# Performance work log

Measured on AMD Instinct MI355X. Metric: run time of the kernel, lower is better.

## Reference

```python
import jax, jax.numpy as jnp
import numpy as np

N = 500000      # examples = M * (nr+1)
K = 20          # context set size (indices[:, 3:])
NR = 24         # negatives per positive
H = 128         # hidden_channels == node feature dim
NODES = 10000   # ingredient vocabulary


def setup_inputs() -> dict:
    key = jax.random.key(0)
    ks = jax.random.split(key, 6)
    indices = jax.random.randint(ks[0], (N, 3 + K), 0, NODES)
    x = jax.random.normal(ks[1], (NODES, H), dtype=jnp.float32)
    scale = 0.02
    W1 = jax.random.normal(ks[2], (H, 3 * H), dtype=jnp.float32) * scale
    b1 = jnp.zeros((H,), jnp.float32)
    W2 = jax.random.normal(ks[3], (H // 2, H), dtype=jnp.float32) * scale
    b2 = jnp.zeros((H // 2,), jnp.float32)
    W3 = jax.random.normal(ks[4], (1, H // 2), dtype=jnp.float32) * scale
    b3 = jnp.zeros((1,), jnp.float32)
    return {"indices": indices, "nr": NR, "x": x,
            "W1": W1, "b1": b1, "W2": W2, "b2": b2, "W3": W3, "b3": b3}


def _embed_context(ctx_idx, x, nr):
    # ctx_idx: [N, K]; one context row per group of (nr+1) examples
    new_idx = ctx_idx[:-1:nr + 1]                 # [M, K]
    emb = x[new_idx]                               # [M, K, H] gather
    s = emb.sum(axis=1)                            # [M, H]
    norm = jnp.maximum((new_idx > 0).sum(axis=1), 1).astype(x.dtype)[:, None]
    mean = s / norm                                # masked mean over context
    return jnp.repeat(mean, nr + 1, axis=0)        # broadcast back to [N, H]


def reference(indices, nr, x, W1, b1, W2, b2, W3, b3):
    ing1 = x[indices[:, 0]]                        # [N, H]
    ing2 = x[indices[:, 1]]                        # [N, H]
    set_emb = _embed_context(indices[:, 3:], x, nr)  # [N, H]
    y = jnp.concatenate([ing1, ing2, set_emb], axis=1)  # [N, 3H]
    y = jax.nn.relu(y @ W1.T + b1)
    y = jax.nn.relu(y @ W2.T + b2)
    return y @ W3.T + b3                           # [N, 1]
```

## Files before the change

### kernel.cpp

```cpp
#include <hip/hip_runtime.h>
#include <hip/hip_bf16.h>

#define N_ROWS   500000
#define NR1      25
#define NGROUPS  20000
#define KCTX     20
#define H        128
#define NODES    10000
#define IDX_COLS 23

#define RPB      128
#define MAXG     7

typedef __attribute__((ext_vector_type(8))) short short8;
typedef __attribute__((ext_vector_type(4))) float f32x4;

__device__ __forceinline__ unsigned pkbf(float lo, float hi) {
  __hip_bfloat162 h = __float22bfloat162_rn(make_float2(lo, hi));
  union { __hip_bfloat162 h; unsigned u; } c; c.h = h;
  return c.u;
}
__device__ __forceinline__ float bf2f(unsigned short u) {
  union { unsigned u; float f; } c; c.u = ((unsigned)u) << 16; return c.f;
}

#define PN 64
#define PRE_BLOCKS ((NODES + PN - 1) / PN)
__global__ __launch_bounds__(256) void k_precompute(
    const float* __restrict__ x, const float* __restrict__ W1,
    const int* __restrict__ indices,
    unsigned short* __restrict__ Pb, int2* __restrict__ idx2) {
  const int tid = threadIdx.x;
  const int m   = blockIdx.y;

  if (m == 3) {
    const int stride = PRE_BLOCKS * 256;
    for (int r = blockIdx.x * 256 + tid; r < N_ROWS; r += stride) {
      idx2[r] = make_int2(indices[(size_t)r * IDX_COLS + 0],
                          indices[(size_t)r * IDX_COLS + 1]);
    }
    return;
  }

  __shared__ short wlds[128][136];
  const int tbase = blockIdx.x * PN;

#pragma unroll
  for (int it = 0; it < 16; ++it) {
    const int f  = it * 256 + tid;
    const int j  = f >> 5;
    const int q4 = f & 31;
    const float4 v = *(const float4*)(W1 + (size_t)j * (3 * H) + m * H + q4 * 4);
    *(unsigned*)&wlds[j][q4 * 4]     = pkbf(v.x, v.y);
    *(unsigned*)&wlds[j][q4 * 4 + 2] = pkbf(v.z, v.w);
  }
  __syncthreads();

  const int lane = tid & 63;
  const int wv   = tid >> 6;
  const int col  = lane & 15;
  const int quad = lane >> 4;

  int node = tbase + wv * 16 + col;
  if (node > NODES - 1) node = NODES - 1;
  const float4* __restrict__ xr = (const float4*)(x + (size_t)node * H);

  short8 Af[4];
#pragma unroll
  for (int kt = 0; kt < 4; ++kt) {
    const int f4 = kt * 8 + quad * 2;
    const float4 v0 = xr[f4], v1 = xr[f4 + 1];
    union { short8 v; unsigned u[4]; } pk;
    pk.u[0] = pkbf(v0.x, v0.y);
    pk.u[1] = pkbf(v0.z, v0.w);
    pk.u[2] = pkbf(v1.x, v1.y);
    pk.u[3] = pkbf(v1.z, v1.w);
    Af[kt] = pk.v;
  }

  f32x4 acc[8];
#pragma unroll
  for (int ct = 0; ct < 8; ++ct) acc[ct] = (f32x4)(0.f);

#pragma unroll
  for (int kt = 0; kt < 4; ++kt) {
#pragma unroll
    for (int ct = 0; ct < 8; ++ct) {
      const short8 Bf = *(const short8*)&wlds[ct * 16 + col][kt * 32 + quad * 8];
      acc[ct] = __builtin_amdgcn_mfma_f32_16x16x32_bf16(Af[kt], Bf, acc[ct], 0, 0, 0);
    }
  }

  unsigned short* __restrict__ Pm = Pb + (size_t)m * NODES * H;
#pragma unroll
  for (int reg = 0; reg < 4; ++reg) {
    const int n = tbase + wv * 16 + quad * 4 + reg;
    if (n < NODES) {
#pragma unroll
      for (int ct = 0; ct < 8; ++ct) {
        union { unsigned u; unsigned short s[2]; } c;
        c.u = pkbf(acc[ct][reg], 0.f);
        Pm[(size_t)n * H + ct * 16 + col] = c.s[0];
      }
    }
  }
}

__global__ __launch_bounds__(256) void k_main(
    const int* __restrict__ indices, const int2* __restrict__ idx2,
    const unsigned short* __restrict__ P1b, const unsigned short* __restrict__ P2b,
    const unsigned short* __restrict__ P3b,
    const float* __restrict__ W2, const float* __restrict__ b1,
    const float* __restrict__ b2, const float* __restrict__ W3,
    const float* __restrict__ b3, float* __restrict__ out) {
  __shared__ short w2s[64][136];
  __shared__ float cgs[MAXG][132];

  const int tid   = threadIdx.x;
  const int rbase = blockIdx.x * RPB;
  const int gbase = rbase / NR1;

  const int lane = tid & 63;
  const int wv   = tid >> 6;
  const int col  = lane & 15;
  const int quad = lane >> 4;

  short8 ua[2][4], ub[2][4];
  int    gl[2];
  {
    const int R = rbase + wv * 32;
#pragma unroll
    for (int rt = 0; rt < 2; ++rt) {
      const int r  = R + rt * 16 + col;
      const int rc = (r < N_ROWS) ? r : (N_ROWS - 1);
      const int2 ii = idx2[rc];
      const short8* __restrict__ pa = (const short8*)(P1b + (size_t)ii.x * H);
      const short8* __restrict__ pb = (const short8*)(P2b + (size_t)ii.y * H);
#pragma unroll
      for (int kt = 0; kt < 4; ++kt) {
        ua[rt][kt] = pa[kt * 4 + quad];
        ub[rt][kt] = pb[kt * 4 + quad];
      }
      gl[rt] = rc / NR1 - gbase;
    }
  }

  for (int idx = tid; idx < 64 * 64; idx += 256) {
    const int n  = idx >> 6;
    const int kp = idx & 63;
    const float2 w = *(const float2*)(W2 + (size_t)n * H + kp * 2);
    *(unsigned*)&w2s[n][kp * 2] = pkbf(w.x, w.y);
  }

  {
    int rlast = rbase + RPB - 1; if (rlast > N_ROWS - 1) rlast = N_ROWS - 1;
    const int G   = rlast / NR1 - gbase + 1;
    const int jj  = (tid & 63) * 2;
    const int sub = tid >> 6;
    const float2 b1v = *(const float2*)(b1 + jj);
#pragma unroll
    for (int it = 0; it < 2; ++it) {
      const int gi = it * 4 + sub;
      if (gi < G) {
        const int* __restrict__ rowidx =
            indices + (size_t)(gbase + gi) * NR1 * IDX_COLS + 3;
        float s0 = 0.f, s1 = 0.f;
        int cnt = 0;
#pragma unroll
        for (int c = 0; c < KCTX; ++c) {
          const int idx = rowidx[c];
          const unsigned w = *(const unsigned*)(P3b + (size_t)idx * H + jj);
          s0 += bf2f((unsigned short)(w & 0xffffu));
          s1 += bf2f((unsigned short)(w >> 16));
          cnt += (idx > 0) ? 1 : 0;
        }
        const float rn = 1.f / (float)((cnt > 1) ? cnt : 1);
        cgs[gi][jj]     = b1v.x + s0 * rn;
        cgs[gi][jj + 1] = b1v.y + s1 * rn;
      }
    }
  }
  __syncthreads();

  float b2v[4], w3v[4];
#pragma unroll
  for (int ct = 0; ct < 4; ++ct) {
    b2v[ct] = b2[ct * 16 + col];
    w3v[ct] = W3[ct * 16 + col];
  }
  const float bias3 = b3[0];

  short8 A[2][4];
#pragma unroll
  for (int rt = 0; rt < 2; ++rt) {
#pragma unroll
    for (int kt = 0; kt < 4; ++kt) {
      union { short8 v; unsigned short s[8]; } va, vb;
      va.v = ua[rt][kt];
      vb.v = ub[rt][kt];
      const float4 c0 = *(const float4*)&cgs[gl[rt]][kt * 32 + quad * 8];
      const float4 c1 = *(const float4*)&cgs[gl[rt]][kt * 32 + quad * 8 + 4];
      const float h0 = fmaxf(bf2f(va.s[0]) + bf2f(vb.s[0]) + c0.x, 0.f);
      const float h1 = fmaxf(bf2f(va.s[1]) + bf2f(vb.s[1]) + c0.y, 0.f);
      const float h2 = fmaxf(bf2f(va.s[2]) + bf2f(vb.s[2]) + c0.z, 0.f);
      const float h3 = fmaxf(bf2f(va.s[3]) + bf2f(vb.s[3]) + c0.w, 0.f);
      const float h4 = fmaxf(bf2f(va.s[4]) + bf2f(vb.s[4]) + c1.x, 0.f);
      const float h5 = fmaxf(bf2f(va.s[5]) + bf2f(vb.s[5]) + c1.y, 0.f);
      const float h6 = fmaxf(bf2f(va.s[6]) + bf2f(vb.s[6]) + c1.z, 0.f);
      const float h7 = fmaxf(bf2f(va.s[7]) + bf2f(vb.s[7]) + c1.w, 0.f);
      union { short8 v; unsigned u[4]; } pk;
      pk.u[0] = pkbf(h0, h1);
      pk.u[1] = pkbf(h2, h3);
      pk.u[2] = pkbf(h4, h5);
      pk.u[3] = pkbf(h6, h7);
      A[rt][kt] = pk.v;
    }
  }

  f32x4 acc[2][4];
#pragma unroll
  for (int rt = 0; rt < 2; ++rt)
#pragma unroll
    for (int ct = 0; ct < 4; ++ct) acc[rt][ct] = (f32x4)(0.f);
#pragma unroll
  for (int kt = 0; kt < 4; ++kt) {
#pragma unroll
    for (int ct = 0; ct < 4; ++ct) {
      const short8 Bf = *(const short8*)&w2s[ct * 16 + col][kt * 32 + quad * 8];
#pragma unroll
      for (int rt = 0; rt < 2; ++rt)
        acc[rt][ct] = __builtin_amdgcn_mfma_f32_16x16x32_bf16(
            A[rt][kt], Bf, acc[rt][ct], 0, 0, 0);
    }
  }

  const int Rt = rbase + wv * 32;
#pragma unroll
  for (int rt = 0; rt < 2; ++rt) {
#pragma unroll
    for (int reg = 0; reg < 4; ++reg) {
      float s = 0.f;
#pragma unroll
      for (int ct = 0; ct < 4; ++ct)
        s += fmaxf(acc[rt][ct][reg] + b2v[ct], 0.f) * w3v[ct];
      s += __shfl_xor(s, 1);
      s += __shfl_xor(s, 2);
      s += __shfl_xor(s, 4);
      s += __shfl_xor(s, 8);
      if (col == 0) {
        const int row = Rt + rt * 16 + quad * 4 + reg;
        if (row < N_ROWS) out[row] = s + bias3;
      }
    }
  }
}

extern "C" void kernel_launch(void* const* d_in, const int* in_sizes, int n_in,
                              void* d_out, int out_size, void* d_ws, size_t ws_size,
                              hipStream_t stream) {
  const int*   indices = (const int*)  d_in[0];
  const float* x  = (const float*)d_in[2];
  const float* W1 = (const float*)d_in[3];
  const float* b1 = (const float*)d_in[4];
  const float* W2 = (const float*)d_in[5];
  const float* b2 = (const float*)d_in[6];
  const float* W3 = (const float*)d_in[7];
  const float* b3 = (const float*)d_in[8];
  float* out = (float*)d_out;

  unsigned short* Pb  = (unsigned short*)d_ws;
  unsigned short* P1b = Pb;
  unsigned short* P2b = Pb + (size_t)NODES * H;
  unsigned short* P3b = Pb + (size_t)2 * NODES * H;
  int2* idx2 = (int2*)(Pb + (size_t)3 * NODES * H);

  dim3 gpre(PRE_BLOCKS, 4);
  k_precompute<<<gpre, 256, 0, stream>>>(x, W1, indices, Pb, idx2);
  k_main<<<(N_ROWS + RPB - 1) / RPB, 256, 0, stream>>>(indices, idx2,
                                                       P1b, P2b, P3b,
                                                       W2, b1, b2, W3, b3, out);
}
```

Before: 170.1 us.

## Precompute per-group context projections in separate kernels instead of per-block gathers

Adds a kernel that computes masked context means from x for each of the 20000 groups. It then projects those means through the third W1 slice (plus b1) in the precompute kernel, splitting that kernel's output columns into two halves across blocks. The main kernel now only loads the precomputed per-group rows instead of re-gathering 20 context rows per group in every block. This removes redundant gathers across overlapping blocks and the bf16 P3 table. The cost is an extra launch and a serial dependency between the means kernel and the precompute kernel.

```diff
diff --git a/kernel.cpp b/kernel.cpp
--- a/kernel.cpp
+++ b/kernel.cpp
@@ -24,33 +24,74 @@
   union { unsigned u; float f; } c; c.u = ((unsigned)u) << 16; return c.f;
 }
 
+#define GPB 8
+#define MEAN_BLOCKS (NGROUPS / GPB)
+__global__ __launch_bounds__(256) void k_means(
+    const int* __restrict__ indices, const float* __restrict__ x,
+    unsigned short* __restrict__ gm) {
+  const int tid = threadIdx.x;
+  const int sub = tid >> 6;
+  const int jj  = (tid & 63) * 2;
+#pragma unroll
+  for (int it = 0; it < GPB / 4; ++it) {
+    const int g = blockIdx.x * GPB + it * 4 + sub;
+    const int* __restrict__ rowidx =
+        indices + (size_t)g * NR1 * IDX_COLS + 3;
+    float s0 = 0.f, s1 = 0.f;
+    int cnt = 0;
+#pragma unroll
+    for (int c = 0; c < KCTX; ++c) {
+      const int idx = rowidx[c];
+      const float2 v = *(const float2*)(x + (size_t)idx * H + jj);
+      s0 += v.x; s1 += v.y;
+      cnt += (idx > 0) ? 1 : 0;
+    }
+    const float rn = 1.f / (float)((cnt > 1) ? cnt : 1);
+    *(unsigned*)(gm + (size_t)g * H + jj) = pkbf(s0 * rn, s1 * rn);
+  }
+}
+
 #define PN 64
-#define PRE_BLOCKS ((NODES + PN - 1) / PN)
+#define PBLK  ((NODES + PN - 1) / PN)
+#define GBLK  ((NGROUPS + PN - 1) / PN)
+#define B_PG  (4 * PBLK)
+#define B_IDX (B_PG + 2 * GBLK)
+#define PRE_BLOCKS (B_IDX + PBLK)
+
 __global__ __launch_bounds__(256) void k_precompute(
     const float* __restrict__ x, const float* __restrict__ W1,
+    const float* __restrict__ b1, const unsigned short* __restrict__ gm,
     const int* __restrict__ indices,
-    unsigned short* __restrict__ Pb, int2* __restrict__ idx2) {
+    unsigned short* __restrict__ Pb, float* __restrict__ Pg,
+    int2* __restrict__ idx2) {
   const int tid = threadIdx.x;
-  const int m   = blockIdx.y;
-
-  if (m == 3) {
-    const int stride = PRE_BLOCKS * 256;
-    for (int r = blockIdx.x * 256 + tid; r < N_ROWS; r += stride) {
+  const int bid = blockIdx.x;
+
+  if (bid >= B_IDX) {
+    const int stride = PBLK * 256;
+    for (int r = (bid - B_IDX) * 256 + tid; r < N_ROWS; r += stride) {
       idx2[r] = make_int2(indices[(size_t)r * IDX_COLS + 0],
                           indices[(size_t)r * IDX_COLS + 1]);
     }
     return;
   }
 
-  __shared__ short wlds[128][136];
-  const int tbase = blockIdx.x * PN;
-
-#pragma unroll
-  for (int it = 0; it < 16; ++it) {
+  __shared__ short wlds[64][136];
+
+  const bool isPg = (bid >= B_PG);
+  int m, sub;
+  if (isPg) { m = 2; sub = bid - B_PG; }
+  else      { m = bid / (2 * PBLK); sub = bid - m * (2 * PBLK); }
+  const int tbase = (sub >> 1) * PN;
+  const int ch    = sub & 1;
+
+#pragma unroll
+  for (int it = 0; it < 8; ++it) {
     const int f  = it * 256 + tid;
     const int j  = f >> 5;
     const int q4 = f & 31;
-    const float4 v = *(const float4*)(W1 + (size_t)j * (3 * H) + m * H + q4 * 4);
+    const float4 v =
+        *(const float4*)(W1 + (size_t)(ch * 64 + j) * (3 * H) + m * H + q4 * 4);
     *(unsigned*)&wlds[j][q4 * 4]     = pkbf(v.x, v.y);
     *(unsigned*)&wlds[j][q4 * 4 + 2] = pkbf(v.z, v.w);
   }
@@ -61,58 +102,80 @@
   const int col  = lane & 15;
   const int quad = lane >> 4;
 
-  int node = tbase + wv * 16 + col;
-  if (node > NODES - 1) node = NODES - 1;
-  const float4* __restrict__ xr = (const float4*)(x + (size_t)node * H);
-
   short8 Af[4];
+  if (isPg) {
+    int g = tbase + wv * 16 + col;
+    if (g > NGROUPS - 1) g = NGROUPS - 1;
+    const short8* __restrict__ gr = (const short8*)(gm + (size_t)g * H);
+#pragma unroll
+    for (int kt = 0; kt < 4; ++kt) Af[kt] = gr[kt * 4 + quad];
+  } else {
+    int node = tbase + wv * 16 + col;
+    if (node > NODES - 1) node = NODES - 1;
+    const float4* __restrict__ xr = (const float4*)(x + (size_t)node * H);
+#pragma unroll
+    for (int kt = 0; kt < 4; ++kt) {
+      const int f4 = kt * 8 + quad * 2;
+      const float4 v0 = xr[f4], v1 = xr[f4 + 1];
+      union { short8 v; unsigned u[4]; } pk;
+      pk.u[0] = pkbf(v0.x, v0.y);
+      pk.u[1] = pkbf(v0.z, v0.w);
+      pk.u[2] = pkbf(v1.x, v1.y);
+      pk.u[3] = pkbf(v1.z, v1.w);
+      Af[kt] = pk.v;
+    }
+  }
+
+  f32x4 acc[4];
+#pragma unroll
+  for (int ct = 0; ct < 4; ++ct) acc[ct] = (f32x4)(0.f);
+
 #pragma unroll
   for (int kt = 0; kt < 4; ++kt) {
-    const int f4 = kt * 8 + quad * 2;
-    const float4 v0 = xr[f4], v1 = xr[f4 + 1];
-    union { short8 v; unsigned u[4]; } pk;
-    pk.u[0] = pkbf(v0.x, v0.y);
-    pk.u[1] = pkbf(v0.z, v0.w);
-    pk.u[2] = pkbf(v1.x, v1.y);
-    pk.u[3] = pkbf(v1.z, v1.w);
-    Af[kt] = pk.v;
-  }
-
-  f32x4 acc[8];
-#pragma unroll
-  for (int ct = 0; ct < 8; ++ct) acc[ct] = (f32x4)(0.f);
-
-#pragma unroll
-  for (int kt = 0; kt < 4; ++kt) {
-#pragma unroll
-    for (int ct = 0; ct < 8; ++ct) {
+#pragma unroll
+    for (int ct = 0; ct < 4; ++ct) {
       const short8 Bf = *(const short8*)&wlds[ct * 16 + col][kt * 32 + quad * 8];
       acc[ct] = __builtin_amdgcn_mfma_f32_16x16x32_bf16(Af[kt], Bf, acc[ct], 0, 0, 0);
     }
   }
 
-  unsigned short* __restrict__ Pm = Pb + (size_t)m * NODES * H;
-#pragma unroll
-  for (int reg = 0; reg < 4; ++reg) {
-    const int n = tbase + wv * 16 + quad * 4 + reg;
-    if (n < NODES) {
-#pragma unroll
-      for (int ct = 0; ct < 8; ++ct) {
-        union { unsigned u; unsigned short s[2]; } c;
-        c.u = pkbf(acc[ct][reg], 0.f);
-        Pm[(size_t)n * H + ct * 16 + col] = c.s[0];
+  if (isPg) {
+    float b1v[4];
+#pragma unroll
+    for (int ct = 0; ct < 4; ++ct) b1v[ct] = b1[ch * 64 + ct * 16 + col];
+#pragma unroll
+    for (int reg = 0; reg < 4; ++reg) {
+      const int g = tbase + wv * 16 + quad * 4 + reg;
+      if (g < NGROUPS) {
+#pragma unroll
+        for (int ct = 0; ct < 4; ++ct)
+          Pg[(size_t)g * H + ch * 64 + ct * 16 + col] = acc[ct][reg] + b1v[ct];
       }
     }
+  } else {
+    unsigned short* __restrict__ Pm = Pb + (size_t)m * NODES * H;
+#pragma unroll
+    for (int reg = 0; reg < 4; ++reg) {
+      const int n = tbase + wv * 16 + quad * 4 + reg;
+      if (n < NODES) {
+#pragma unroll
+        for (int ct = 0; ct < 4; ++ct) {
+          union { unsigned u; unsigned short s[2]; } c;
+          c.u = pkbf(acc[ct][reg], 0.f);
+          Pm[(size_t)n * H + ch * 64 + ct * 16 + col] = c.s[0];
+        }
+      }
+    }
   }
 }
 
 __global__ __launch_bounds__(256) void k_main(
-    const int* __restrict__ indices, const int2* __restrict__ idx2,
+    const int2* __restrict__ idx2,
     const unsigned short* __restrict__ P1b, const unsigned short* __restrict__ P2b,
-    const unsigned short* __restrict__ P3b,
-    const float* __restrict__ W2, const float* __restrict__ b1,
-    const float* __restrict__ b2, const float* __restrict__ W3,
-    const float* __restrict__ b3, float* __restrict__ out) {
+    const float* __restrict__ Pg,
+    const float* __restrict__ W2, const float* __restrict__ b2,
+    const float* __restrict__ W3, const float* __restrict__ b3,
+    float* __restrict__ out) {
   __shared__ short w2s[64][136];
   __shared__ float cgs[MAXG][132];
 
@@ -154,30 +217,12 @@
 
   {
     int rlast = rbase + RPB - 1; if (rlast > N_ROWS - 1) rlast = N_ROWS - 1;
-    const int G   = rlast / NR1 - gbase + 1;
-    const int jj  = (tid & 63) * 2;
-    const int sub = tid >> 6;
-    const float2 b1v = *(const float2*)(b1 + jj);
-#pragma unroll
-    for (int it = 0; it < 2; ++it) {
-      const int gi = it * 4 + sub;
-      if (gi < G) {
-        const int* __restrict__ rowidx =
-            indices + (size_t)(gbase + gi) * NR1 * IDX_COLS + 3;
-        float s0 = 0.f, s1 = 0.f;
-        int cnt = 0;
-#pragma unroll
-        for (int c = 0; c < KCTX; ++c) {
-          const int idx = rowidx[c];
-          const unsigned w = *(const unsigned*)(P3b + (size_t)idx * H + jj);
-          s0 += bf2f((unsigned short)(w & 0xffffu));
-          s1 += bf2f((unsigned short)(w >> 16));
-          cnt += (idx > 0) ? 1 : 0;
-        }
-        const float rn = 1.f / (float)((cnt > 1) ? cnt : 1);
-        cgs[gi][jj]     = b1v.x + s0 * rn;
-        cgs[gi][jj + 1] = b1v.y + s1 * rn;
-      }
+    const int G = rlast / NR1 - gbase + 1;
+    const float* __restrict__ Pgrow = Pg + (size_t)gbase * H;
+    for (int i = tid; i < G * 32; i += 256) {
+      const int g = i >> 5;
+      const int c = (i & 31) * 4;
+      *(float4*)&cgs[g][c] = *(const float4*)(Pgrow + (size_t)g * H + c);
     }
   }
   __syncthreads();
@@ -271,12 +316,13 @@
   unsigned short* Pb  = (unsigned short*)d_ws;
   unsigned short* P1b = Pb;
   unsigned short* P2b = Pb + (size_t)NODES * H;
-  unsigned short* P3b = Pb + (size_t)2 * NODES * H;
-  int2* idx2 = (int2*)(Pb + (size_t)3 * NODES * H);
-
-  dim3 gpre(PRE_BLOCKS, 4);
-  k_precompute<<<gpre, 256, 0, stream>>>(x, W1, indices, Pb, idx2);
-  k_main<<<(N_ROWS + RPB - 1) / RPB, 256, 0, stream>>>(indices, idx2,
-                                                       P1b, P2b, P3b,
-                                                       W2, b1, b2, W3, b3, out);
-}
+  unsigned short* gm  = Pb + (size_t)2 * NODES * H;
+  float* Pg   = (float*)(gm + (size_t)NGROUPS * H);
+  int2*  idx2 = (int2*)(Pg + (size_t)NGROUPS * H);
+
+  k_means<<<MEAN_BLOCKS, 256, 0, stream>>>(indices, x, gm);
+  k_precompute<<<PRE_BLOCKS, 256, 0, stream>>>(x, W1, b1, gm, indices,
+                                               Pb, Pg, idx2);
+  k_main<<<(N_ROWS + RPB - 1) / RPB, 256, 0, stream>>>(idx2, P1b, P2b, Pg,
+                                                       W2, b2, W3, b3, out);
+}
```

Result: slower. 177.7 us (+4.5%).
